# Performance work log

Measured on AMD Instinct MI355X. Metric: run time of the kernel, lower is better.

The kernel has to match this reference:

```python
import jax, jax.numpy as jnp
import numpy as np

B, T, H, S, K, V = 64, 2048, 512, 512, 128, 128
EPS = 1e-12  # F.normalize default eps


def setup_inputs() -> dict:
    key = jax.random.key(0)
    ks = jax.random.split(key, 9)
    scale_s = 1.0 / np.sqrt(S)
    scale_h = 1.0 / np.sqrt(H)
    return {
        "decoder_state": jax.random.normal(ks[0], (B, S), jnp.float32),
        "listener_output": jax.random.normal(ks[1], (B, T, H), jnp.float32),
        "outputs_length": jax.random.randint(ks[2], (B,), 1, T + 1, jnp.int32),
        "Ws": jax.random.uniform(ks[3], (K, S), jnp.float32, -scale_s, scale_s),
        "bs": jax.random.uniform(ks[4], (K,), jnp.float32, -scale_s, scale_s),
        "Wh": jax.random.uniform(ks[5], (K, H), jnp.float32, -scale_h, scale_h),
        "bh": jax.random.uniform(ks[6], (K,), jnp.float32, -scale_h, scale_h),
        "Wv": jax.random.uniform(ks[7], (V, H), jnp.float32, -scale_h, scale_h),
        "bv": jax.random.uniform(ks[8], (V,), jnp.float32, -scale_h, scale_h),
    }


def reference(decoder_state, listener_output, outputs_length, Ws, bs, Wh, bh, Wv, bv):
    # query: (B, K); key: (B, T, K)
    query = decoder_state @ Ws.T + bs
    keys = jnp.einsum('bth,kh->btk', listener_output, Wh) + bh
    energy = jnp.einsum('bk,btk->bt', query, keys)          # (B, T)
    attention = jax.nn.softmax(energy, axis=-1)
    # mask: positions >= outputs_length[i] zeroed, EXCEPT sample i == 0 (original loop skips i==0)
    t_idx = jnp.arange(T)
    valid = t_idx[None, :] < outputs_length[:, None]        # (B, T)
    valid = valid.at[0].set(True)
    mask = valid.astype(attention.dtype)
    attention = attention * mask
    # L1 normalize over time (F.normalize p=1, dim=2)
    denom = jnp.maximum(jnp.sum(jnp.abs(attention), axis=-1, keepdims=True), EPS)
    attention = attention / denom
    value = jnp.einsum('bth,vh->btv', listener_output, Wv) + bv  # (B, T, V)
    value = value * mask[:, :, None]
    context = jnp.einsum('bt,btv->bv', attention, value)     # (B, V)
    return context, attention[:, None, :]
```

## Files before the change

### kernel.cpp

```cpp
#include <hip/hip_runtime.h>
#include <hip/hip_bf16.h>

#define B 64
#define T 2048
#define H 512
#define S 512
#define K 128
#define V 128
#define SPL 32
#define RPB (T / SPL)
#define RPW (RPB / 4)
#define PSTRIDE 516

__global__ __launch_bounds__(256) void prep_kernel(
    const float* __restrict__ dec, const float* __restrict__ Ws,
    const float* __restrict__ bs, const float* __restrict__ Wh,
    const float* __restrict__ bh, float* __restrict__ wq,
    float* __restrict__ cb) {
  const int b = blockIdx.x;
  const int tid = threadIdx.x;
  __shared__ float s_dec[S];
  __shared__ float s_q[K];

  for (int i = tid; i < S; i += 256) s_dec[i] = dec[b * S + i];
  __syncthreads();

  if (tid < K) {
    const float* w = Ws + (size_t)tid * S;
    float a0 = 0.f, a1 = 0.f, a2 = 0.f, a3 = 0.f;
    for (int s = 0; s < S; s += 16) {
      const float4 w0 = *(const float4*)(w + s);
      const float4 w1 = *(const float4*)(w + s + 4);
      const float4 w2 = *(const float4*)(w + s + 8);
      const float4 w3 = *(const float4*)(w + s + 12);
      const float4 d0 = *(const float4*)(s_dec + s);
      const float4 d1 = *(const float4*)(s_dec + s + 4);
      const float4 d2 = *(const float4*)(s_dec + s + 8);
      const float4 d3 = *(const float4*)(s_dec + s + 12);
      a0 += w0.x * d0.x + w0.y * d0.y + w0.z * d0.z + w0.w * d0.w;
      a1 += w1.x * d1.x + w1.y * d1.y + w1.z * d1.z + w1.w * d1.w;
      a2 += w2.x * d2.x + w2.y * d2.y + w2.z * d2.z + w2.w * d2.w;
      a3 += w3.x * d3.x + w3.y * d3.y + w3.z * d3.z + w3.w * d3.w;
    }
    s_q[tid] = bs[tid] + ((a0 + a1) + (a2 + a3));
  }
  __syncthreads();

  if (tid < 64) {
    float c = s_q[tid] * bh[tid] + s_q[tid + 64] * bh[tid + 64];
    #pragma unroll
    for (int off = 32; off > 0; off >>= 1) c += __shfl_xor(c, off);
    if (tid == 0) cb[b] = c;
  }

  for (int h = tid; h < H; h += 256) {
    float a0 = 0.f, a1 = 0.f, a2 = 0.f, a3 = 0.f;
    #pragma unroll 8
    for (int k = 0; k < K; k += 4) {
      a0 += s_q[k]     * Wh[(size_t)k * H + h];
      a1 += s_q[k + 1] * Wh[(size_t)(k + 1) * H + h];
      a2 += s_q[k + 2] * Wh[(size_t)(k + 2) * H + h];
      a3 += s_q[k + 3] * Wh[(size_t)(k + 3) * H + h];
    }
    wq[b * H + h] = (a0 + a1) + (a2 + a3);
  }
}

__global__ __launch_bounds__(256) void fused_kernel(
    const float* __restrict__ L, const float* __restrict__ wq,
    const float* __restrict__ cb, const int* __restrict__ len,
    float* __restrict__ energy, float* __restrict__ partials) {
  const int b = blockIdx.x >> 5;
  const int sp = blockIdx.x & (SPL - 1);
  const int lane = threadIdx.x & 63;
  const int wave = threadIdx.x >> 6;
  const int tid = threadIdx.x;
  const int lb = (b == 0) ? T : len[b];

  __shared__ float s_ctx[4][H];
  __shared__ float s_ml[4][2];

  const int h0 = lane * 4;
  float m = -__builtin_huge_valf();
  float lsum = 0.f;
  float4 acc0 = {0.f, 0.f, 0.f, 0.f};
  float4 acc1 = {0.f, 0.f, 0.f, 0.f};

  const int start = sp * RPB + wave * RPW;
  const int end = min(start + RPW, lb);

  if (start < end) {
    const float4 q0 = *(const float4*)(wq + b * H + h0);
    const float4 q1 = *(const float4*)(wq + b * H + 256 + h0);
    const float c = cb[b];
    const float* Lr = L + ((size_t)b * T + start) * H;
    int r = start;
    for (; r + 3 < end; r += 4, Lr += 4 * H) {
      const float4 r0a = *(const float4*)(Lr + h0);
      const float4 r0b = *(const float4*)(Lr + 256 + h0);
      const float4 r1a = *(const float4*)(Lr + H + h0);
      const float4 r1b = *(const float4*)(Lr + H + 256 + h0);
      const float4 r2a = *(const float4*)(Lr + 2 * H + h0);
      const float4 r2b = *(const float4*)(Lr + 2 * H + 256 + h0);
      const float4 r3a = *(const float4*)(Lr + 3 * H + h0);
      const float4 r3b = *(const float4*)(Lr + 3 * H + 256 + h0);
      float d0 = r0a.x * q0.x + r0a.y * q0.y + r0a.z * q0.z + r0a.w * q0.w +
                 r0b.x * q1.x + r0b.y * q1.y + r0b.z * q1.z + r0b.w * q1.w;
      float d1 = r1a.x * q0.x + r1a.y * q0.y + r1a.z * q0.z + r1a.w * q0.w +
                 r1b.x * q1.x + r1b.y * q1.y + r1b.z * q1.z + r1b.w * q1.w;
      float d2 = r2a.x * q0.x + r2a.y * q0.y + r2a.z * q0.z + r2a.w * q0.w +
                 r2b.x * q1.x + r2b.y * q1.y + r2b.z * q1.z + r2b.w * q1.w;
      float d3 = r3a.x * q0.x + r3a.y * q0.y + r3a.z * q0.z + r3a.w * q0.w +
                 r3b.x * q1.x + r3b.y * q1.y + r3b.z * q1.z + r3b.w * q1.w;
      #pragma unroll
      for (int off = 32; off > 0; off >>= 1) {
        d0 += __shfl_xor(d0, off);
        d1 += __shfl_xor(d1, off);
        d2 += __shfl_xor(d2, off);
        d3 += __shfl_xor(d3, off);
      }
      const float e0 = d0 + c;
      const float e1 = d1 + c;
      const float e2 = d2 + c;
      const float e3 = d3 + c;
      if (lane == 0) {
        *(float4*)(energy + b * T + r) = make_float4(e0, e1, e2, e3);
      }
      const float mx = fmaxf(fmaxf(e0, e1), fmaxf(e2, e3));
      const float mn = fmaxf(m, mx);
      const float s = __expf(m - mn);
      const float w0 = __expf(e0 - mn);
      const float w1 = __expf(e1 - mn);
      const float w2 = __expf(e2 - mn);
      const float w3 = __expf(e3 - mn);
      m = mn;
      lsum = lsum * s + ((w0 + w1) + (w2 + w3));
      acc0.x = acc0.x * s + ((w0 * r0a.x + w1 * r1a.x) + (w2 * r2a.x + w3 * r3a.x));
      acc0.y = acc0.y * s + ((w0 * r0a.y + w1 * r1a.y) + (w2 * r2a.y + w3 * r3a.y));
      acc0.z = acc0.z * s + ((w0 * r0a.z + w1 * r1a.z) + (w2 * r2a.z + w3 * r3a.z));
      acc0.w = acc0.w * s + ((w0 * r0a.w + w1 * r1a.w) + (w2 * r2a.w + w3 * r3a.w));
      acc1.x = acc1.x * s + ((w0 * r0b.x + w1 * r1b.x) + (w2 * r2b.x + w3 * r3b.x));
      acc1.y = acc1.y * s + ((w0 * r0b.y + w1 * r1b.y) + (w2 * r2b.y + w3 * r3b.y));
      acc1.z = acc1.z * s + ((w0 * r0b.z + w1 * r1b.z) + (w2 * r2b.z + w3 * r3b.z));
      acc1.w = acc1.w * s + ((w0 * r0b.w + w1 * r1b.w) + (w2 * r2b.w + w3 * r3b.w));
    }
    for (; r < end; ++r, Lr += H) {
      const float4 a0 = *(const float4*)(Lr + h0);
      const float4 a1 = *(const float4*)(Lr + 256 + h0);
      float d = a0.x * q0.x + a0.y * q0.y + a0.z * q0.z + a0.w * q0.w +
                a1.x * q1.x + a1.y * q1.y + a1.z * q1.z + a1.w * q1.w;
      #pragma unroll
      for (int off = 32; off > 0; off >>= 1) d += __shfl_xor(d, off);
      const float e = d + c;
      if (lane == 0) energy[b * T + r] = e;
      const float mn = fmaxf(m, e);
      const float s = __expf(m - mn);
      const float w = __expf(e - mn);
      m = mn;
      lsum = lsum * s + w;
      acc0.x = acc0.x * s + w * a0.x;
      acc0.y = acc0.y * s + w * a0.y;
      acc0.z = acc0.z * s + w * a0.z;
      acc0.w = acc0.w * s + w * a0.w;
      acc1.x = acc1.x * s + w * a1.x;
      acc1.y = acc1.y * s + w * a1.y;
      acc1.z = acc1.z * s + w * a1.z;
      acc1.w = acc1.w * s + w * a1.w;
    }
  }

  if (lane == 0) { s_ml[wave][0] = m; s_ml[wave][1] = lsum; }
  *(float4*)&s_ctx[wave][h0] = acc0;
  *(float4*)&s_ctx[wave][256 + h0] = acc1;
  __syncthreads();

  const float M = fmaxf(fmaxf(s_ml[0][0], s_ml[1][0]),
                        fmaxf(s_ml[2][0], s_ml[3][0]));
  float sc[4], ltot = 0.f;
  #pragma unroll
  for (int w = 0; w < 4; w++) {
    sc[w] = (s_ml[w][0] > -1e38f) ? __expf(s_ml[w][0] - M) : 0.f;
    ltot += s_ml[w][1] * sc[w];
  }
  float v0 = 0.f, v1 = 0.f;
  #pragma unroll
  for (int w = 0; w < 4; w++) {
    v0 += s_ctx[w][tid * 2] * sc[w];
    v1 += s_ctx[w][tid * 2 + 1] * sc[w];
  }
  float* part = partials + (size_t)blockIdx.x * PSTRIDE;
  *(float2*)(part + tid * 2) = make_float2(v0, v1);
  if (tid == 0) { part[512] = M; part[513] = ltot; }
}

__global__ __launch_bounds__(256) void combine_kernel(
    const float* __restrict__ partials, const float* __restrict__ Wv,
    const float* __restrict__ bv, const float* __restrict__ energy,
    const int* __restrict__ len, float* __restrict__ ctx_out,
    float* __restrict__ att) {
  const int b = blockIdx.x;
  const int tid = threadIdx.x;
  __shared__ float s_ml[SPL][2];
  __shared__ float s_ctx[H];

  if (tid < SPL) {
    const float* p = partials + (size_t)(b * SPL + tid) * PSTRIDE;
    s_ml[tid][0] = p[512];
    s_ml[tid][1] = p[513];
  }
  __syncthreads();

  float M = -__builtin_huge_valf();
  #pragma unroll
  for (int sp = 0; sp < SPL; sp++) M = fmaxf(M, s_ml[sp][0]);
  float ltot = 0.f;
  #pragma unroll
  for (int sp = 0; sp < SPL; sp++) {
    const float s = (s_ml[sp][0] > -1e38f) ? __expf(s_ml[sp][0] - M) : 0.f;
    ltot += s_ml[sp][1] * s;
  }
  const float inv = 1.0f / fmaxf(ltot, 1e-12f);

  float v0 = 0.f, v1 = 0.f;
  #pragma unroll 4
  for (int sp = 0; sp < SPL; sp++) {
    const float s = (s_ml[sp][0] > -1e38f) ? __expf(s_ml[sp][0] - M) : 0.f;
    const float* p = partials + (size_t)(b * SPL + sp) * PSTRIDE;
    v0 += p[tid * 2] * s;
    v1 += p[tid * 2 + 1] * s;
  }
  s_ctx[tid * 2] = v0 * inv;
  s_ctx[tid * 2 + 1] = v1 * inv;
  __syncthreads();

  const int lb = (b == 0) ? T : len[b];
  #pragma unroll
  for (int i = 0; i < 8; i++) {
    const int t = tid + 256 * i;
    const float e = (t < lb) ? energy[b * T + t] : M;
    att[b * T + t] = (t < lb) ? __expf(e - M) * inv : 0.f;
  }

  if (tid < V) {
    const float* w = Wv + (size_t)tid * H;
    float a0 = bv[tid], a1 = 0.f, a2 = 0.f, a3 = 0.f;
    for (int h = 0; h < H; h += 16) {
      a0 += w[h]      * s_ctx[h]      + w[h + 1]  * s_ctx[h + 1] +
            w[h + 2]  * s_ctx[h + 2]  + w[h + 3]  * s_ctx[h + 3];
      a1 += w[h + 4]  * s_ctx[h + 4]  + w[h + 5]  * s_ctx[h + 5] +
            w[h + 6]  * s_ctx[h + 6]  + w[h + 7]  * s_ctx[h + 7];
      a2 += w[h + 8]  * s_ctx[h + 8]  + w[h + 9]  * s_ctx[h + 9] +
            w[h + 10] * s_ctx[h + 10] + w[h + 11] * s_ctx[h + 11];
      a3 += w[h + 12] * s_ctx[h + 12] + w[h + 13] * s_ctx[h + 13] +
            w[h + 14] * s_ctx[h + 14] + w[h + 15] * s_ctx[h + 15];
    }
    ctx_out[b * V + tid] = (a0 + a1) + (a2 + a3);
  }
}

extern "C" void kernel_launch(void* const* d_in, const int* in_sizes, int n_in,
                              void* d_out, int out_size, void* d_ws,
                              size_t ws_size, hipStream_t stream) {
  const float* dec = (const float*)d_in[0];
  const float* L   = (const float*)d_in[1];
  const int*   len = (const int*)d_in[2];
  const float* Ws  = (const float*)d_in[3];
  const float* bs  = (const float*)d_in[4];
  const float* Wh  = (const float*)d_in[5];
  const float* bh  = (const float*)d_in[6];
  const float* Wv  = (const float*)d_in[7];
  const float* bv  = (const float*)d_in[8];

  float* ctx_out = (float*)d_out;
  float* att_out = (float*)d_out + B * V;

  float* ws = (float*)d_ws;
  float* wq = ws;
  float* cb = wq + B * H;
  float* energy = cb + B;
  float* partials = energy + B * T;

  prep_kernel<<<B, 256, 0, stream>>>(dec, Ws, bs, Wh, bh, wq, cb);
  fused_kernel<<<B * SPL, 256, 0, stream>>>(L, wq, cb, len, energy, partials);
  combine_kernel<<<B, 256, 0, stream>>>(partials, Wv, bv, energy, len,
                                        ctx_out, att_out);
}
```

Baseline: 389.5 us.

## Fuse combine into main kernel via last-block atomic counter; skip idle block reductions

Removes the separate combine kernel: each split block publishes its partial, bumps a per-batch atomic counter, and the last arriving block performs the final softmax merge, attention write and Wv projection. Blocks entirely past the sequence length skip the intra-block reduction and write only a sentinel. The prep kernel resets the counters and its Wh·q loop is rewritten with more independent accumulators per thread. This saves a launch and the gap between kernels, at the cost of a fence plus atomic per block and a serialized tail on the last block of each batch.

Result: slower. 854.3 us (+119.3%).

```diff
diff --git a/kernel.cpp b/kernel.cpp
--- a/kernel.cpp
+++ b/kernel.cpp
@@ -1,5 +1,4 @@
 #include <hip/hip_runtime.h>
-#include <hip/hip_bf16.h>
 
 #define B 64
 #define T 2048
@@ -16,11 +15,13 @@
     const float* __restrict__ dec, const float* __restrict__ Ws,
     const float* __restrict__ bs, const float* __restrict__ Wh,
     const float* __restrict__ bh, float* __restrict__ wq,
-    float* __restrict__ cb) {
+    float* __restrict__ cb, int* __restrict__ cnt) {
   const int b = blockIdx.x;
   const int tid = threadIdx.x;
   __shared__ float s_dec[S];
   __shared__ float s_q[K];
+
+  if (tid == 0) cnt[b] = 0;
 
   for (int i = tid; i < S; i += 256) s_dec[i] = dec[b * S + i];
   __syncthreads();
@@ -53,23 +54,39 @@
     if (tid == 0) cb[b] = c;
   }
 
-  for (int h = tid; h < H; h += 256) {
+  {
+    const float* W = Wh + tid;
     float a0 = 0.f, a1 = 0.f, a2 = 0.f, a3 = 0.f;
-    #pragma unroll 8
-    for (int k = 0; k < K; k += 4) {
-      a0 += s_q[k]     * Wh[(size_t)k * H + h];
-      a1 += s_q[k + 1] * Wh[(size_t)(k + 1) * H + h];
-      a2 += s_q[k + 2] * Wh[(size_t)(k + 2) * H + h];
-      a3 += s_q[k + 3] * Wh[(size_t)(k + 3) * H + h];
-    }
-    wq[b * H + h] = (a0 + a1) + (a2 + a3);
+    float a4 = 0.f, a5 = 0.f, a6 = 0.f, a7 = 0.f;
+    float c0 = 0.f, c1 = 0.f, c2 = 0.f, c3 = 0.f;
+    float c4 = 0.f, c5 = 0.f, c6 = 0.f, c7 = 0.f;
+    for (int k = 0; k < K; k += 8) {
+      const float q0 = s_q[k],     q1 = s_q[k + 1];
+      const float q2 = s_q[k + 2], q3 = s_q[k + 3];
+      const float q4 = s_q[k + 4], q5 = s_q[k + 5];
+      const float q6 = s_q[k + 6], q7 = s_q[k + 7];
+      const float* Wk = W + (size_t)k * H;
+      a0 += q0 * Wk[0 * H];       c0 += q0 * Wk[0 * H + 256];
+      a1 += q1 * Wk[1 * H];       c1 += q1 * Wk[1 * H + 256];
+      a2 += q2 * Wk[2 * H];       c2 += q2 * Wk[2 * H + 256];
+      a3 += q3 * Wk[3 * H];       c3 += q3 * Wk[3 * H + 256];
+      a4 += q4 * Wk[4 * H];       c4 += q4 * Wk[4 * H + 256];
+      a5 += q5 * Wk[5 * H];       c5 += q5 * Wk[5 * H + 256];
+      a6 += q6 * Wk[6 * H];       c6 += q6 * Wk[6 * H + 256];
+      a7 += q7 * Wk[7 * H];       c7 += q7 * Wk[7 * H + 256];
+    }
+    wq[b * H + tid] = (((a0 + a1) + (a2 + a3)) + ((a4 + a5) + (a6 + a7)));
+    wq[b * H + tid + 256] = (((c0 + c1) + (c2 + c3)) + ((c4 + c5) + (c6 + c7)));
   }
 }
 
 __global__ __launch_bounds__(256) void fused_kernel(
     const float* __restrict__ L, const float* __restrict__ wq,
     const float* __restrict__ cb, const int* __restrict__ len,
-    float* __restrict__ energy, float* __restrict__ partials) {
+    const float* __restrict__ Wv, const float* __restrict__ bv,
+    float* __restrict__ energy, float* __restrict__ partials,
+    int* __restrict__ cnt, float* __restrict__ ctx_out,
+    float* __restrict__ att) {
   const int b = blockIdx.x >> 5;
   const int sp = blockIdx.x & (SPL - 1);
   const int lane = threadIdx.x & 63;
@@ -79,6 +96,7 @@
 
   __shared__ float s_ctx[4][H];
   __shared__ float s_ml[4][2];
+  __shared__ int s_ret;
 
   const int h0 = lane * 4;
   float m = -__builtin_huge_valf();
@@ -88,6 +106,7 @@
 
   const int start = sp * RPB + wave * RPW;
   const int end = min(start + RPW, lb);
+  const bool block_busy = (sp * RPB < lb);
 
   if (start < end) {
     const float4 q0 = *(const float4*)(wq + b * H + h0);
@@ -169,90 +188,93 @@
     }
   }
 
-  if (lane == 0) { s_ml[wave][0] = m; s_ml[wave][1] = lsum; }
-  *(float4*)&s_ctx[wave][h0] = acc0;
-  *(float4*)&s_ctx[wave][256 + h0] = acc1;
-  __syncthreads();
-
-  const float M = fmaxf(fmaxf(s_ml[0][0], s_ml[1][0]),
-                        fmaxf(s_ml[2][0], s_ml[3][0]));
-  float sc[4], ltot = 0.f;
-  #pragma unroll
-  for (int w = 0; w < 4; w++) {
-    sc[w] = (s_ml[w][0] > -1e38f) ? __expf(s_ml[w][0] - M) : 0.f;
-    ltot += s_ml[w][1] * sc[w];
-  }
-  float v0 = 0.f, v1 = 0.f;
-  #pragma unroll
-  for (int w = 0; w < 4; w++) {
-    v0 += s_ctx[w][tid * 2] * sc[w];
-    v1 += s_ctx[w][tid * 2 + 1] * sc[w];
-  }
   float* part = partials + (size_t)blockIdx.x * PSTRIDE;
-  *(float2*)(part + tid * 2) = make_float2(v0, v1);
-  if (tid == 0) { part[512] = M; part[513] = ltot; }
-}
-
-__global__ __launch_bounds__(256) void combine_kernel(
-    const float* __restrict__ partials, const float* __restrict__ Wv,
-    const float* __restrict__ bv, const float* __restrict__ energy,
-    const int* __restrict__ len, float* __restrict__ ctx_out,
-    float* __restrict__ att) {
-  const int b = blockIdx.x;
-  const int tid = threadIdx.x;
-  __shared__ float s_ml[SPL][2];
-  __shared__ float s_ctx[H];
-
+  if (block_busy) {
+    if (lane == 0) { s_ml[wave][0] = m; s_ml[wave][1] = lsum; }
+    *(float4*)&s_ctx[wave][h0] = acc0;
+    *(float4*)&s_ctx[wave][256 + h0] = acc1;
+    __syncthreads();
+
+    const float M = fmaxf(fmaxf(s_ml[0][0], s_ml[1][0]),
+                          fmaxf(s_ml[2][0], s_ml[3][0]));
+    float sc[4], ltot = 0.f;
+    #pragma unroll
+    for (int w = 0; w < 4; w++) {
+      sc[w] = (s_ml[w][0] > -1e38f) ? __expf(s_ml[w][0] - M) : 0.f;
+      ltot += s_ml[w][1] * sc[w];
+    }
+    float v0 = 0.f, v1 = 0.f;
+    #pragma unroll
+    for (int w = 0; w < 4; w++) {
+      v0 += s_ctx[w][tid * 2] * sc[w];
+      v1 += s_ctx[w][tid * 2 + 1] * sc[w];
+    }
+    *(float2*)(part + tid * 2) = make_float2(v0, v1);
+    if (tid == 0) { part[512] = M; part[513] = ltot; }
+  } else {
+    if (tid == 0) { part[512] = -__builtin_huge_valf(); part[513] = 0.f; }
+  }
+
+  __threadfence();
+  __syncthreads();
+  if (tid == 0) {
+    s_ret = __hip_atomic_fetch_add(&cnt[b], 1, __ATOMIC_ACQ_REL,
+                                   __HIP_MEMORY_SCOPE_AGENT);
+  }
+  __syncthreads();
+  if (s_ret != SPL - 1) return;
+
+  __shared__ float s_mlc[SPL][2];
+  __shared__ float s_cf[H];
   if (tid < SPL) {
     const float* p = partials + (size_t)(b * SPL + tid) * PSTRIDE;
-    s_ml[tid][0] = p[512];
-    s_ml[tid][1] = p[513];
-  }
-  __syncthreads();
-
-  float M = -__builtin_huge_valf();
+    s_mlc[tid][0] = p[512];
+    s_mlc[tid][1] = p[513];
+  }
+  __syncthreads();
+
+  float Mg = -__builtin_huge_valf();
   #pragma unroll
-  for (int sp = 0; sp < SPL; sp++) M = fmaxf(M, s_ml[sp][0]);
-  float ltot = 0.f;
+  for (int sp2 = 0; sp2 < SPL; sp2++) Mg = fmaxf(Mg, s_mlc[sp2][0]);
+  float ltg = 0.f;
   #pragma unroll
-  for (int sp = 0; sp < SPL; sp++) {
-    const float s = (s_ml[sp][0] > -1e38f) ? __expf(s_ml[sp][0] - M) : 0.f;
-    ltot += s_ml[sp][1] * s;
-  }
-  const float inv = 1.0f / fmaxf(ltot, 1e-12f);
+  for (int sp2 = 0; sp2 < SPL; sp2++) {
+    if (s_mlc[sp2][0] > -1e38f) ltg += s_mlc[sp2][1] * __expf(s_mlc[sp2][0] - Mg);
+  }
+  const float inv = 1.0f / fmaxf(ltg, 1e-12f);
 
   float v0 = 0.f, v1 = 0.f;
-  #pragma unroll 4
-  for (int sp = 0; sp < SPL; sp++) {
-    const float s = (s_ml[sp][0] > -1e38f) ? __expf(s_ml[sp][0] - M) : 0.f;
-    const float* p = partials + (size_t)(b * SPL + sp) * PSTRIDE;
-    v0 += p[tid * 2] * s;
-    v1 += p[tid * 2 + 1] * s;
-  }
-  s_ctx[tid * 2] = v0 * inv;
-  s_ctx[tid * 2 + 1] = v1 * inv;
-  __syncthreads();
-
-  const int lb = (b == 0) ? T : len[b];
+  for (int sp2 = 0; sp2 < SPL; sp2++) {
+    if (s_mlc[sp2][0] > -1e38f) {
+      const float s = __expf(s_mlc[sp2][0] - Mg);
+      const float* p = partials + (size_t)(b * SPL + sp2) * PSTRIDE;
+      v0 += p[tid * 2] * s;
+      v1 += p[tid * 2 + 1] * s;
+    }
+  }
+  s_cf[tid * 2] = v0 * inv;
+  s_cf[tid * 2 + 1] = v1 * inv;
+  __syncthreads();
+
   #pragma unroll
   for (int i = 0; i < 8; i++) {
     const int t = tid + 256 * i;
-    const float e = (t < lb) ? energy[b * T + t] : M;
-    att[b * T + t] = (t < lb) ? __expf(e - M) * inv : 0.f;
+    const float e = (t < lb) ? energy[b * T + t] : Mg;
+    att[b * T + t] = (t < lb) ? __expf(e - Mg) * inv : 0.f;
   }
 
   if (tid < V) {
     const float* w = Wv + (size_t)tid * H;
     float a0 = bv[tid], a1 = 0.f, a2 = 0.f, a3 = 0.f;
     for (int h = 0; h < H; h += 16) {
-      a0 += w[h]      * s_ctx[h]      + w[h + 1]  * s_ctx[h + 1] +
-            w[h + 2]  * s_ctx[h + 2]  + w[h + 3]  * s_ctx[h + 3];
-      a1 += w[h + 4]  * s_ctx[h + 4]  + w[h + 5]  * s_ctx[h + 5] +
-            w[h + 6]  * s_ctx[h + 6]  + w[h + 7]  * s_ctx[h + 7];
-      a2 += w[h + 8]  * s_ctx[h + 8]  + w[h + 9]  * s_ctx[h + 9] +
-            w[h + 10] * s_ctx[h + 10] + w[h + 11] * s_ctx[h + 11];
-      a3 += w[h + 12] * s_ctx[h + 12] + w[h + 13] * s_ctx[h + 13] +
-            w[h + 14] * s_ctx[h + 14] + w[h + 15] * s_ctx[h + 15];
+      a0 += w[h]      * s_cf[h]      + w[h + 1]  * s_cf[h + 1] +
+            w[h + 2]  * s_cf[h + 2]  + w[h + 3]  * s_cf[h + 3];
+      a1 += w[h + 4]  * s_cf[h + 4]  + w[h + 5]  * s_cf[h + 5] +
+            w[h + 6]  * s_cf[h + 6]  + w[h + 7]  * s_cf[h + 7];
+      a2 += w[h + 8]  * s_cf[h + 8]  + w[h + 9]  * s_cf[h + 9] +
+            w[h + 10] * s_cf[h + 10] + w[h + 11] * s_cf[h + 11];
+      a3 += w[h + 12] * s_cf[h + 12] + w[h + 13] * s_cf[h + 13] +
+            w[h + 14] * s_cf[h + 14] + w[h + 15] * s_cf[h + 15];
     }
     ctx_out[b * V + tid] = (a0 + a1) + (a2 + a3);
   }
@@ -279,9 +301,9 @@
   float* cb = wq + B * H;
   float* energy = cb + B;
   float* partials = energy + B * T;
-
-  prep_kernel<<<B, 256, 0, stream>>>(dec, Ws, bs, Wh, bh, wq, cb);
-  fused_kernel<<<B * SPL, 256, 0, stream>>>(L, wq, cb, len, energy, partials);
-  combine_kernel<<<B, 256, 0, stream>>>(partials, Wv, bv, energy, len,
-                                        ctx_out, att_out);
+  int* cnt = (int*)(partials + B * SPL * PSTRIDE);
+
+  prep_kernel<<<B, 256, 0, stream>>>(dec, Ws, bs, Wh, bh, wq, cb, cnt);
+  fused_kernel<<<B * SPL, 256, 0, stream>>>(L, wq, cb, len, Wv, bv, energy,
+                                            partials, cnt, ctx_out, att_out);
 }
```

## Prefetch next row group in fused loop and skip empty-split partial work

Applied to the files above, without the earlier changes.

The fused attention loop now double-buffers its register loads, fetching the next four rows of listener_output while computing the current four, to hide global memory latency. Splits lying entirely past the sequence length skip the shared-memory reduction and write only a sentinel (-inf max, zero sum). The combine kernel then skips loading partials for those empty splits. The prep kernel's Wh projection is unrolled over eight k values with two h outputs per thread. The prefetch roughly doubles the live float4 registers in the loop, which could lower occupancy.

New measurement: 392.9 us. No clear change (+0.9%).

```diff
diff --git a/kernel.cpp b/kernel.cpp
--- a/kernel.cpp
+++ b/kernel.cpp
@@ -1,5 +1,4 @@
 #include <hip/hip_runtime.h>
-#include <hip/hip_bf16.h>
 
 #define B 64
 #define T 2048
@@ -53,16 +52,29 @@
     if (tid == 0) cb[b] = c;
   }
 
-  for (int h = tid; h < H; h += 256) {
+  {
+    const float* W = Wh + tid;
     float a0 = 0.f, a1 = 0.f, a2 = 0.f, a3 = 0.f;
-    #pragma unroll 8
-    for (int k = 0; k < K; k += 4) {
-      a0 += s_q[k]     * Wh[(size_t)k * H + h];
-      a1 += s_q[k + 1] * Wh[(size_t)(k + 1) * H + h];
-      a2 += s_q[k + 2] * Wh[(size_t)(k + 2) * H + h];
-      a3 += s_q[k + 3] * Wh[(size_t)(k + 3) * H + h];
-    }
-    wq[b * H + h] = (a0 + a1) + (a2 + a3);
+    float a4 = 0.f, a5 = 0.f, a6 = 0.f, a7 = 0.f;
+    float c0 = 0.f, c1 = 0.f, c2 = 0.f, c3 = 0.f;
+    float c4 = 0.f, c5 = 0.f, c6 = 0.f, c7 = 0.f;
+    for (int k = 0; k < K; k += 8) {
+      const float q0 = s_q[k],     q1 = s_q[k + 1];
+      const float q2 = s_q[k + 2], q3 = s_q[k + 3];
+      const float q4 = s_q[k + 4], q5 = s_q[k + 5];
+      const float q6 = s_q[k + 6], q7 = s_q[k + 7];
+      const float* Wk = W + (size_t)k * H;
+      a0 += q0 * Wk[0 * H];       c0 += q0 * Wk[0 * H + 256];
+      a1 += q1 * Wk[1 * H];       c1 += q1 * Wk[1 * H + 256];
+      a2 += q2 * Wk[2 * H];       c2 += q2 * Wk[2 * H + 256];
+      a3 += q3 * Wk[3 * H];       c3 += q3 * Wk[3 * H + 256];
+      a4 += q4 * Wk[4 * H];       c4 += q4 * Wk[4 * H + 256];
+      a5 += q5 * Wk[5 * H];       c5 += q5 * Wk[5 * H + 256];
+      a6 += q6 * Wk[6 * H];       c6 += q6 * Wk[6 * H + 256];
+      a7 += q7 * Wk[7 * H];       c7 += q7 * Wk[7 * H + 256];
+    }
+    wq[b * H + tid] = (((a0 + a1) + (a2 + a3)) + ((a4 + a5) + (a6 + a7)));
+    wq[b * H + tid + 256] = (((c0 + c1) + (c2 + c3)) + ((c4 + c5) + (c6 + c7)));
   }
 }
 
@@ -88,6 +100,7 @@
 
   const int start = sp * RPB + wave * RPW;
   const int end = min(start + RPW, lb);
+  const bool block_busy = (sp * RPB < lb);
 
   if (start < end) {
     const float4 q0 = *(const float4*)(wq + b * H + h0);
@@ -95,23 +108,40 @@
     const float c = cb[b];
     const float* Lr = L + ((size_t)b * T + start) * H;
     int r = start;
-    for (; r + 3 < end; r += 4, Lr += 4 * H) {
-      const float4 r0a = *(const float4*)(Lr + h0);
-      const float4 r0b = *(const float4*)(Lr + 256 + h0);
-      const float4 r1a = *(const float4*)(Lr + H + h0);
-      const float4 r1b = *(const float4*)(Lr + H + 256 + h0);
-      const float4 r2a = *(const float4*)(Lr + 2 * H + h0);
-      const float4 r2b = *(const float4*)(Lr + 2 * H + 256 + h0);
-      const float4 r3a = *(const float4*)(Lr + 3 * H + h0);
-      const float4 r3b = *(const float4*)(Lr + 3 * H + 256 + h0);
-      float d0 = r0a.x * q0.x + r0a.y * q0.y + r0a.z * q0.z + r0a.w * q0.w +
-                 r0b.x * q1.x + r0b.y * q1.y + r0b.z * q1.z + r0b.w * q1.w;
-      float d1 = r1a.x * q0.x + r1a.y * q0.y + r1a.z * q0.z + r1a.w * q0.w +
-                 r1b.x * q1.x + r1b.y * q1.y + r1b.z * q1.z + r1b.w * q1.w;
-      float d2 = r2a.x * q0.x + r2a.y * q0.y + r2a.z * q0.z + r2a.w * q0.w +
-                 r2b.x * q1.x + r2b.y * q1.y + r2b.z * q1.z + r2b.w * q1.w;
-      float d3 = r3a.x * q0.x + r3a.y * q0.y + r3a.z * q0.z + r3a.w * q0.w +
-                 r3b.x * q1.x + r3b.y * q1.y + r3b.z * q1.z + r3b.w * q1.w;
+
+    float4 c0a, c0b, c1a, c1b, c2a, c2b, c3a, c3b;
+    if (r + 3 < end) {
+      c0a = *(const float4*)(Lr + h0);
+      c0b = *(const float4*)(Lr + 256 + h0);
+      c1a = *(const float4*)(Lr + H + h0);
+      c1b = *(const float4*)(Lr + H + 256 + h0);
+      c2a = *(const float4*)(Lr + 2 * H + h0);
+      c2b = *(const float4*)(Lr + 2 * H + 256 + h0);
+      c3a = *(const float4*)(Lr + 3 * H + h0);
+      c3b = *(const float4*)(Lr + 3 * H + 256 + h0);
+    }
+    for (; r + 3 < end; ) {
+      const float* Ln = Lr + 4 * H;
+      const bool has_next = (r + 7 < end);
+      float4 n0a, n0b, n1a, n1b, n2a, n2b, n3a, n3b;
+      if (has_next) {
+        n0a = *(const float4*)(Ln + h0);
+        n0b = *(const float4*)(Ln + 256 + h0);
+        n1a = *(const float4*)(Ln + H + h0);
+        n1b = *(const float4*)(Ln + H + 256 + h0);
+        n2a = *(const float4*)(Ln + 2 * H + h0);
+        n2b = *(const float4*)(Ln + 2 * H + 256 + h0);
+        n3a = *(const float4*)(Ln + 3 * H + h0);
+        n3b = *(const float4*)(Ln + 3 * H + 256 + h0);
+      }
+      float d0 = c0a.x * q0.x + c0a.y * q0.y + c0a.z * q0.z + c0a.w * q0.w +
+                 c0b.x * q1.x + c0b.y * q1.y + c0b.z * q1.z + c0b.w * q1.w;
+      float d1 = c1a.x * q0.x + c1a.y * q0.y + c1a.z * q0.z + c1a.w * q0.w +
+                 c1b.x * q1.x + c1b.y * q1.y + c1b.z * q1.z + c1b.w * q1.w;
+      float d2 = c2a.x * q0.x + c2a.y * q0.y + c2a.z * q0.z + c2a.w * q0.w +
+                 c2b.x * q1.x + c2b.y * q1.y + c2b.z * q1.z + c2b.w * q1.w;
+      float d3 = c3a.x * q0.x + c3a.y * q0.y + c3a.z * q0.z + c3a.w * q0.w +
+                 c3b.x * q1.x + c3b.y * q1.y + c3b.z * q1.z + c3b.w * q1.w;
       #pragma unroll
       for (int off = 32; off > 0; off >>= 1) {
         d0 += __shfl_xor(d0, off);
@@ -135,14 +165,20 @@
       const float w3 = __expf(e3 - mn);
       m = mn;
       lsum = lsum * s + ((w0 + w1) + (w2 + w3));
-      acc0.x = acc0.x * s + ((w0 * r0a.x + w1 * r1a.x) + (w2 * r2a.x + w3 * r3a.x));
-      acc0.y = acc0.y * s + ((w0 * r0a.y + w1 * r1a.y) + (w2 * r2a.y + w3 * r3a.y));
-      acc0.z = acc0.z * s + ((w0 * r0a.z + w1 * r1a.z) + (w2 * r2a.z + w3 * r3a.z));
-      acc0.w = acc0.w * s + ((w0 * r0a.w + w1 * r1a.w) + (w2 * r2a.w + w3 * r3a.w));
-      acc1.x = acc1.x * s + ((w0 * r0b.x + w1 * r1b.x) + (w2 * r2b.x + w3 * r3b.x));
-      acc1.y = acc1.y * s + ((w0 * r0b.y + w1 * r1b.y) + (w2 * r2b.y + w3 * r3b.y));
-      acc1.z = acc1.z * s + ((w0 * r0b.z + w1 * r1b.z) + (w2 * r2b.z + w3 * r3b.z));
-      acc1.w = acc1.w * s + ((w0 * r0b.w + w1 * r1b.w) + (w2 * r2b.w + w3 * r3b.w));
+      acc0.x = acc0.x * s + ((w0 * c0a.x + w1 * c1a.x) + (w2 * c2a.x + w3 * c3a.x));
+      acc0.y = acc0.y * s + ((w0 * c0a.y + w1 * c1a.y) + (w2 * c2a.y + w3 * c3a.y));
+      acc0.z = acc0.z * s + ((w0 * c0a.z + w1 * c1a.z) + (w2 * c2a.z + w3 * c3a.z));
+      acc0.w = acc0.w * s + ((w0 * c0a.w + w1 * c1a.w) + (w2 * c2a.w + w3 * c3a.w));
+      acc1.x = acc1.x * s + ((w0 * c0b.x + w1 * c1b.x) + (w2 * c2b.x + w3 * c3b.x));
+      acc1.y = acc1.y * s + ((w0 * c0b.y + w1 * c1b.y) + (w2 * c2b.y + w3 * c3b.y));
+      acc1.z = acc1.z * s + ((w0 * c0b.z + w1 * c1b.z) + (w2 * c2b.z + w3 * c3b.z));
+      acc1.w = acc1.w * s + ((w0 * c0b.w + w1 * c1b.w) + (w2 * c2b.w + w3 * c3b.w));
+      r += 4;
+      Lr = Ln;
+      if (has_next) {
+        c0a = n0a; c0b = n0b; c1a = n1a; c1b = n1b;
+        c2a = n2a; c2b = n2b; c3a = n3a; c3b = n3b;
+      }
     }
     for (; r < end; ++r, Lr += H) {
       const float4 a0 = *(const float4*)(Lr + h0);
@@ -169,28 +205,32 @@
     }
   }
 
-  if (lane == 0) { s_ml[wave][0] = m; s_ml[wave][1] = lsum; }
-  *(float4*)&s_ctx[wave][h0] = acc0;
-  *(float4*)&s_ctx[wave][256 + h0] = acc1;
-  __syncthreads();
-
-  const float M = fmaxf(fmaxf(s_ml[0][0], s_ml[1][0]),
-                        fmaxf(s_ml[2][0], s_ml[3][0]));
-  float sc[4], ltot = 0.f;
-  #pragma unroll
-  for (int w = 0; w < 4; w++) {
-    sc[w] = (s_ml[w][0] > -1e38f) ? __expf(s_ml[w][0] - M) : 0.f;
-    ltot += s_ml[w][1] * sc[w];
-  }
-  float v0 = 0.f, v1 = 0.f;
-  #pragma unroll
-  for (int w = 0; w < 4; w++) {
-    v0 += s_ctx[w][tid * 2] * sc[w];
-    v1 += s_ctx[w][tid * 2 + 1] * sc[w];
-  }
   float* part = partials + (size_t)blockIdx.x * PSTRIDE;
-  *(float2*)(part + tid * 2) = make_float2(v0, v1);
-  if (tid == 0) { part[512] = M; part[513] = ltot; }
+  if (block_busy) {
+    if (lane == 0) { s_ml[wave][0] = m; s_ml[wave][1] = lsum; }
+    *(float4*)&s_ctx[wave][h0] = acc0;
+    *(float4*)&s_ctx[wave][256 + h0] = acc1;
+    __syncthreads();
+
+    const float M = fmaxf(fmaxf(s_ml[0][0], s_ml[1][0]),
+                          fmaxf(s_ml[2][0], s_ml[3][0]));
+    float sc[4], ltot = 0.f;
+    #pragma unroll
+    for (int w = 0; w < 4; w++) {
+      sc[w] = (s_ml[w][0] > -1e38f) ? __expf(s_ml[w][0] - M) : 0.f;
+      ltot += s_ml[w][1] * sc[w];
+    }
+    float v0 = 0.f, v1 = 0.f;
+    #pragma unroll
+    for (int w = 0; w < 4; w++) {
+      v0 += s_ctx[w][tid * 2] * sc[w];
+      v1 += s_ctx[w][tid * 2 + 1] * sc[w];
+    }
+    *(float2*)(part + tid * 2) = make_float2(v0, v1);
+    if (tid == 0) { part[512] = M; part[513] = ltot; }
+  } else {
+    if (tid == 0) { part[512] = -__builtin_huge_valf(); part[513] = 0.f; }
+  }
 }
 
 __global__ __launch_bounds__(256) void combine_kernel(
@@ -216,18 +256,18 @@
   float ltot = 0.f;
   #pragma unroll
   for (int sp = 0; sp < SPL; sp++) {
-    const float s = (s_ml[sp][0] > -1e38f) ? __expf(s_ml[sp][0] - M) : 0.f;
-    ltot += s_ml[sp][1] * s;
+    if (s_ml[sp][0] > -1e38f) ltot += s_ml[sp][1] * __expf(s_ml[sp][0] - M);
   }
   const float inv = 1.0f / fmaxf(ltot, 1e-12f);
 
   float v0 = 0.f, v1 = 0.f;
-  #pragma unroll 4
   for (int sp = 0; sp < SPL; sp++) {
-    const float s = (s_ml[sp][0] > -1e38f) ? __expf(s_ml[sp][0] - M) : 0.f;
-    const float* p = partials + (size_t)(b * SPL + sp) * PSTRIDE;
-    v0 += p[tid * 2] * s;
-    v1 += p[tid * 2 + 1] * s;
+    if (s_ml[sp][0] > -1e38f) {
+      const float s = __expf(s_ml[sp][0] - M);
+      const float* p = partials + (size_t)(b * SPL + sp) * PSTRIDE;
+      v0 += p[tid * 2] * s;
+      v1 += p[tid * 2 + 1] * s;
+    }
   }
   s_ctx[tid * 2] = v0 * inv;
   s_ctx[tid * 2 + 1] = v1 * inv;
```

## Split prep across blocks, halve attention splits, skip idle block reductions

Applied to the files above, without the earlier changes.

The prep kernel is split four ways per batch row, so each block computes a quarter of the Wh projection, which raises the block count from 64 to 256. Each block still recomputes the query itself. The fused kernel uses 16 splits instead of 32, so each block handles twice as many rows. Blocks with no valid rows now skip the shared-memory reduction and write only a sentinel. The combine kernel skips empty partials and fully unrolls its loop. Fewer splits cut partial traffic and launch overhead but also reduce parallelism in the memory-bound main kernel.

Measured after the change: 390.9 us. Within noise of the previous version (+0.4%).

```diff
diff --git a/kernel.cpp b/kernel.cpp
--- a/kernel.cpp
+++ b/kernel.cpp
@@ -1,5 +1,4 @@
 #include <hip/hip_runtime.h>
-#include <hip/hip_bf16.h>
 
 #define B 64
 #define T 2048
@@ -7,17 +6,19 @@
 #define S 512
 #define K 128
 #define V 128
-#define SPL 32
+#define SPL 16
 #define RPB (T / SPL)
 #define RPW (RPB / 4)
 #define PSTRIDE 516
+#define PREP_SPLIT 4
 
 __global__ __launch_bounds__(256) void prep_kernel(
     const float* __restrict__ dec, const float* __restrict__ Ws,
     const float* __restrict__ bs, const float* __restrict__ Wh,
     const float* __restrict__ bh, float* __restrict__ wq,
     float* __restrict__ cb) {
-  const int b = blockIdx.x;
+  const int b = blockIdx.x >> 2;
+  const int part = blockIdx.x & (PREP_SPLIT - 1);
   const int tid = threadIdx.x;
   __shared__ float s_dec[S];
   __shared__ float s_q[K];
@@ -46,23 +47,30 @@
   }
   __syncthreads();
 
-  if (tid < 64) {
+  if (part == 0 && tid < 64) {
     float c = s_q[tid] * bh[tid] + s_q[tid + 64] * bh[tid + 64];
     #pragma unroll
     for (int off = 32; off > 0; off >>= 1) c += __shfl_xor(c, off);
     if (tid == 0) cb[b] = c;
   }
 
-  for (int h = tid; h < H; h += 256) {
+  if (tid < 128) {
+    const int h = part * 128 + tid;
+    const float* W = Wh + h;
     float a0 = 0.f, a1 = 0.f, a2 = 0.f, a3 = 0.f;
-    #pragma unroll 8
-    for (int k = 0; k < K; k += 4) {
-      a0 += s_q[k]     * Wh[(size_t)k * H + h];
-      a1 += s_q[k + 1] * Wh[(size_t)(k + 1) * H + h];
-      a2 += s_q[k + 2] * Wh[(size_t)(k + 2) * H + h];
-      a3 += s_q[k + 3] * Wh[(size_t)(k + 3) * H + h];
-    }
-    wq[b * H + h] = (a0 + a1) + (a2 + a3);
+    float a4 = 0.f, a5 = 0.f, a6 = 0.f, a7 = 0.f;
+    for (int k = 0; k < K; k += 8) {
+      const float* Wk = W + (size_t)k * H;
+      a0 += s_q[k]     * Wk[0 * H];
+      a1 += s_q[k + 1] * Wk[1 * H];
+      a2 += s_q[k + 2] * Wk[2 * H];
+      a3 += s_q[k + 3] * Wk[3 * H];
+      a4 += s_q[k + 4] * Wk[4 * H];
+      a5 += s_q[k + 5] * Wk[5 * H];
+      a6 += s_q[k + 6] * Wk[6 * H];
+      a7 += s_q[k + 7] * Wk[7 * H];
+    }
+    wq[b * H + h] = (((a0 + a1) + (a2 + a3)) + ((a4 + a5) + (a6 + a7)));
   }
 }
 
@@ -70,7 +78,7 @@
     const float* __restrict__ L, const float* __restrict__ wq,
     const float* __restrict__ cb, const int* __restrict__ len,
     float* __restrict__ energy, float* __restrict__ partials) {
-  const int b = blockIdx.x >> 5;
+  const int b = blockIdx.x >> 4;
   const int sp = blockIdx.x & (SPL - 1);
   const int lane = threadIdx.x & 63;
   const int wave = threadIdx.x >> 6;
@@ -88,6 +96,7 @@
 
   const int start = sp * RPB + wave * RPW;
   const int end = min(start + RPW, lb);
+  const bool block_busy = (sp * RPB < lb);
 
   if (start < end) {
     const float4 q0 = *(const float4*)(wq + b * H + h0);
@@ -169,28 +178,32 @@
     }
   }
 
-  if (lane == 0) { s_ml[wave][0] = m; s_ml[wave][1] = lsum; }
-  *(float4*)&s_ctx[wave][h0] = acc0;
-  *(float4*)&s_ctx[wave][256 + h0] = acc1;
-  __syncthreads();
-
-  const float M = fmaxf(fmaxf(s_ml[0][0], s_ml[1][0]),
-                        fmaxf(s_ml[2][0], s_ml[3][0]));
-  float sc[4], ltot = 0.f;
-  #pragma unroll
-  for (int w = 0; w < 4; w++) {
-    sc[w] = (s_ml[w][0] > -1e38f) ? __expf(s_ml[w][0] - M) : 0.f;
-    ltot += s_ml[w][1] * sc[w];
-  }
-  float v0 = 0.f, v1 = 0.f;
-  #pragma unroll
-  for (int w = 0; w < 4; w++) {
-    v0 += s_ctx[w][tid * 2] * sc[w];
-    v1 += s_ctx[w][tid * 2 + 1] * sc[w];
-  }
   float* part = partials + (size_t)blockIdx.x * PSTRIDE;
-  *(float2*)(part + tid * 2) = make_float2(v0, v1);
-  if (tid == 0) { part[512] = M; part[513] = ltot; }
+  if (block_busy) {
+    if (lane == 0) { s_ml[wave][0] = m; s_ml[wave][1] = lsum; }
+    *(float4*)&s_ctx[wave][h0] = acc0;
+    *(float4*)&s_ctx[wave][256 + h0] = acc1;
+    __syncthreads();
+
+    const float M = fmaxf(fmaxf(s_ml[0][0], s_ml[1][0]),
+                          fmaxf(s_ml[2][0], s_ml[3][0]));
+    float sc[4], ltot = 0.f;
+    #pragma unroll
+    for (int w = 0; w < 4; w++) {
+      sc[w] = (s_ml[w][0] > -1e38f) ? __expf(s_ml[w][0] - M) : 0.f;
+      ltot += s_ml[w][1] * sc[w];
+    }
+    float v0 = 0.f, v1 = 0.f;
+    #pragma unroll
+    for (int w = 0; w < 4; w++) {
+      v0 += s_ctx[w][tid * 2] * sc[w];
+      v1 += s_ctx[w][tid * 2 + 1] * sc[w];
+    }
+    *(float2*)(part + tid * 2) = make_float2(v0, v1);
+    if (tid == 0) { part[512] = M; part[513] = ltot; }
+  } else {
+    if (tid == 0) { part[512] = -__builtin_huge_valf(); part[513] = 0.f; }
+  }
 }
 
 __global__ __launch_bounds__(256) void combine_kernel(
@@ -216,18 +229,19 @@
   float ltot = 0.f;
   #pragma unroll
   for (int sp = 0; sp < SPL; sp++) {
-    const float s = (s_ml[sp][0] > -1e38f) ? __expf(s_ml[sp][0] - M) : 0.f;
-    ltot += s_ml[sp][1] * s;
+    if (s_ml[sp][0] > -1e38f) ltot += s_ml[sp][1] * __expf(s_ml[sp][0] - M);
   }
   const float inv = 1.0f / fmaxf(ltot, 1e-12f);
 
   float v0 = 0.f, v1 = 0.f;
-  #pragma unroll 4
+  #pragma unroll
   for (int sp = 0; sp < SPL; sp++) {
-    const float s = (s_ml[sp][0] > -1e38f) ? __expf(s_ml[sp][0] - M) : 0.f;
-    const float* p = partials + (size_t)(b * SPL + sp) * PSTRIDE;
-    v0 += p[tid * 2] * s;
-    v1 += p[tid * 2 + 1] * s;
+    if (s_ml[sp][0] > -1e38f) {
+      const float s = __expf(s_ml[sp][0] - M);
+      const float* p = partials + (size_t)(b * SPL + sp) * PSTRIDE;
+      v0 += p[tid * 2] * s;
+      v1 += p[tid * 2 + 1] * s;
+    }
   }
   s_ctx[tid * 2] = v0 * inv;
   s_ctx[tid * 2 + 1] = v1 * inv;
@@ -280,7 +294,7 @@
   float* energy = cb + B;
   float* partials = energy + B * T;
 
-  prep_kernel<<<B, 256, 0, stream>>>(dec, Ws, bs, Wh, bh, wq, cb);
+  prep_kernel<<<B * PREP_SPLIT, 256, 0, stream>>>(dec, Ws, bs, Wh, bh, wq, cb);
   fused_kernel<<<B * SPL, 256, 0, stream>>>(L, wq, cb, len, energy, partials);
   combine_kernel<<<B, 256, 0, stream>>>(partials, Wv, bv, energy, len,
                                         ctx_out, att_out);
```
